# Kernel optimization log

Measured on AMD Instinct MI355X. Metric: run time of the kernel, lower is better.

The kernel has to match this reference:

```python
import jax, jax.numpy as jnp
import numpy as np

B, T, D, S, H = 512, 365, 16, 32, 256


def setup_inputs() -> dict:
    key = jax.random.key(0)
    ks = jax.random.split(key, 16)
    sc = 0.05
    rn = lambda k, shp: sc * jax.random.normal(k, shp, dtype=jnp.float32)
    return {
        "x": jax.random.normal(ks[0], (B, T, D), dtype=jnp.float32),
        "x_static": jax.random.normal(ks[1], (B, S), dtype=jnp.float32),
        # layer 0 LSTM params (PyTorch layout: [4H, in], gate order i,f,g,o)
        "Wih0": rn(ks[2], (4 * H, D)),
        "Whh0": rn(ks[3], (4 * H, H)),
        "bih0": rn(ks[4], (4 * H,)),
        "bhh0": rn(ks[5], (4 * H,)),
        # layer 1 LSTM params
        "Wih1": rn(ks[6], (4 * H, H)),
        "Whh1": rn(ks[7], (4 * H, H)),
        "bih1": rn(ks[8], (4 * H,)),
        "bhh1": rn(ks[9], (4 * H,)),
        # static_to_hidden Linear
        "Ws": rn(ks[10], (H, S)),
        "bs": rn(ks[11], (H,)),
        # output Linear (H -> 1)
        "Wo": rn(ks[12], (1, H)),
        "bo": rn(ks[13], (1,)),
    }


def _lstm_layer(x, h0, c0, Wih, Whh, bih, bhh):
    # Precompute input contribution as one big GEMM: [B,T,4H]
    xg = jnp.einsum('btd,gd->btg', x, Wih) + (bih + bhh)

    def step(carry, xt):
        h, c = carry
        g = xt + h @ Whh.T                      # [B,4H]
        i, f, gg, o = jnp.split(g, 4, axis=-1)  # PyTorch gate order i,f,g,o
        i = jax.nn.sigmoid(i)
        f = jax.nn.sigmoid(f)
        gg = jnp.tanh(gg)
        o = jax.nn.sigmoid(o)
        c = f * c + i * gg
        h = o * jnp.tanh(c)
        return (h, c), h

    (_, _), hs = jax.lax.scan(step, (h0, c0), jnp.swapaxes(xg, 0, 1))  # hs: [T,B,H]
    return jnp.swapaxes(hs, 0, 1)  # [B,T,H]


def reference(x, x_static, Wih0, Whh0, bih0, bhh0, Wih1, Whh1, bih1, bhh1, Ws, bs, Wo, bo):
    # h0 = c0 = static projection, shared across layers (repeat over num_layers)
    h0 = x_static @ Ws.T + bs                       # [B,H]
    y = _lstm_layer(x, h0, h0, Wih0, Whh0, bih0, bhh0)
    y = _lstm_layer(y, h0, h0, Wih1, Whh1, bih1, bhh1)
    out = (y @ Wo.T + bo)[..., 0]                   # [B,T]
    return out
```

## Files before the change

### kernel.cpp

```cpp
#include <hip/hip_runtime.h>

#define TT 365
#define BB 512
#define DD 16
#define HH 256
#define SS 32

typedef __attribute__((ext_vector_type(8))) short short8;
typedef __attribute__((ext_vector_type(4))) float f32x4;
typedef __attribute__((ext_vector_type(4))) unsigned u32x4;
typedef unsigned long long u64;

#define SENT 0x7FC07FC07FC07FC0ULL
#define TMASK64 0x4000400040004000ULL

__device__ __host__ inline short f2bf(float f){
  union { float f; unsigned u; } v; v.f = f;
  unsigned r = v.u + 0x7FFFu + ((v.u >> 16) & 1u);
  return (short)(r >> 16);
}
__device__ inline float sigm(float x){ return 1.0f/(1.0f+__expf(-x)); }
__device__ inline float tanhx(float x){ return 2.0f/(1.0f+__expf(-2.0f*x)) - 1.0f; }

__device__ inline unsigned cvtpk(float a, float b){
  unsigned r;
  asm("v_cvt_pk_bf16_f32 %0, %1, %2" : "=v"(r) : "v"(a), "v"(b));
  return r;
}

__device__ inline int fragAddr(int k, int m){
  return ((k>>5)*512) + ((((k&31)>>3)*16 + m)*8) + (k&7);
}

__device__ inline void pub_store(u64* p, u64 v){
  asm volatile("global_store_dwordx2 %0, %1, off sc0 sc1"
               :: "v"(p), "v"(v) : "memory");
}

#define RAW_BAR() do{ \
    asm volatile("s_waitcnt lgkmcnt(0)\n\ts_barrier" ::: "memory"); \
    __builtin_amdgcn_sched_barrier(0); }while(0)

__global__ void prep_weights(const float* __restrict__ Wih0, const float* __restrict__ Whh0,
                             const float* __restrict__ Wih1, const float* __restrict__ Whh1,
                             short* __restrict__ Wb0, short* __restrict__ Wb1)
{
  int idx = blockIdx.x*blockDim.x + threadIdx.x;
  const int n0 = 16*36*512;
  const int n1 = 16*64*512;
  if (idx < n0){
    int frag = idx >> 9, pos = idx & 511;
    int lane = pos >> 3, jj = pos & 7;
    int slot = frag / 36, rem = frag % 36;
    int ks = rem >> 2, nt = rem & 3;
    int n = nt*256 + slot*16 + (lane & 15);
    float v = 0.0f;
    if (ks == 0){
      int k32 = (lane>>4)*8 + jj;
      if (k32 < 16) v = Wih0[n*16 + k32];
    } else {
      int k = (ks-1)*32 + (lane>>4)*8 + jj;
      v = Whh0[n*256 + k];
    }
    Wb0[idx] = f2bf(v);
  } else if (idx < n0 + n1){
    int e = idx - n0;
    int frag = e >> 9, pos = e & 511;
    int lane = pos >> 3, jj = pos & 7;
    int slot = frag >> 6, rem = frag & 63;
    int ks = rem >> 2, nt = rem & 3;
    int n = nt*256 + slot*16 + (lane & 15);
    int k = ks*32 + (lane>>4)*8 + jj;
    float v = (k < 256) ? Wih1[n*256 + k] : Whh1[n*256 + (k-256)];
    Wb1[e] = f2bf(v);
  }
}

__global__ void prep_h0(const float* __restrict__ xs, const float* __restrict__ Ws,
                        const float* __restrict__ bs, float* __restrict__ h0init)
{
  int i = blockIdx.x*blockDim.x + threadIdx.x;
  int b = i >> 8, jj = i & 255;
  float s = bs[jj];
  const float* xr = xs + b*SS;
  const float* wr = Ws + jj*SS;
#pragma unroll
  for (int q=0;q<SS;++q) s += xr[q]*wr[q];
  h0init[i] = s;
}

__global__ void prep_bias(const float* __restrict__ a0, const float* __restrict__ a1,
                          const float* __restrict__ a2, const float* __restrict__ a3,
                          float* __restrict__ b0o, float* __restrict__ b1o)
{
  int i = threadIdx.x + blockIdx.x*blockDim.x;
  if (i < 1024) b0o[i] = a0[i] + a1[i];
  else if (i < 2048) b1o[i-1024] = a2[i-1024] + a3[i-1024];
}

__global__ void prep_zero(float* __restrict__ out, u64* __restrict__ ring)
{
  int i = blockIdx.x*blockDim.x + threadIdx.x;
  if (i < BB*TT) out[i] = 0.0f;
  if (i < 131072) ring[i] = SENT;
}

__global__ __launch_bounds__(256, 1) void lstm_fused(
    const short* __restrict__ Wb0, const short* __restrict__ Wb1,
    const float* __restrict__ h0i, const float* __restrict__ b0c,
    const float* __restrict__ b1c, const float* __restrict__ x,
    const float* __restrict__ Wo, const float* __restrict__ bo,
    u64* __restrict__ ring, float* __restrict__ out)
{
  __shared__ alignas(16) short AX[2][512];
  __shared__ alignas(16) short AH0[2][4096];
  __shared__ alignas(16) short AH1[4096];
  __shared__ float outacc[2][16][4];

  const int tid  = threadIdx.x;
  const int w    = tid >> 6;
  const int lane = tid & 63;
  const int col16= lane & 15;
  const int quad = lane >> 4;
  const int c    = blockIdx.x >> 5;
  const int g    = blockIdx.x & 31;
  const int rowbase = g * 16;
  const int slot = c*4 + w;
  const int colg = slot*16 + col16;

  short8 F0[36], F1[64];
  {
    const short8* p0 = (const short8*)Wb0 + slot*36*64 + lane;
#pragma unroll
    for (int f=0; f<36; ++f) F0[f] = p0[f*64];
    const short8* p1 = (const short8*)Wb1 + slot*64*64 + lane;
#pragma unroll
    for (int f=0; f<64; ++f) F1[f] = p1[f*64];
  }
  float bia0[4], bia1[4];
#pragma unroll
  for (int nt=0; nt<4; ++nt){
    bia0[nt] = b0c[nt*256 + slot*16 + col16];
    bia1[nt] = b1c[nt*256 + slot*16 + col16];
  }
  const float wo = Wo[colg];
  const float bos = bo[0];

  float c0[4], c1[4];
#pragma unroll
  for (int r=0; r<4; ++r){
    c0[r] = h0i[(rowbase + quad*4 + r)*HH + colg];
    c1[r] = c0[r];
  }
  for (int i = tid; i < 4096; i += 256){
    int m = i >> 8, k = i & 255;
    short v = f2bf(h0i[(rowbase+m)*HH + k]);
    int a = fragAddr(k,m);
    AH0[0][a] = v;
    AH1[a]    = v;
  }
  {
    int m = tid >> 4, d = tid & 15;
    AX[0][fragAddr(d, m)] = f2bf(x[(rowbase+m)*TT*DD + d]);
    AX[0][fragAddr(16 + d, m)] = 0;
    AX[1][fragAddr(16 + d, m)] = 0;
  }
  __syncthreads();

  const f32x4 zero = {0.0f,0.0f,0.0f,0.0f};
  const int qd = tid & 3;
  const int cl = (tid >> 2) & 63;
  const int ka = (((c + 1) & 3) << 6) + cl;
  const int kb = (((c + 2) & 3) << 6) + cl;
  const int kc = (((c + 3) & 3) << 6) + cl;

  u64 pv1_prev = 0;

#define CHKW(tv,dst,fl,TG) do{ u64 _t=(tv); \
    if(!(fl) && ((_t & TMASK64)==(TG))){ (dst)=_t & ~TMASK64; (fl)=true; } }while(0)

  for (int s=0; s<=TT; ++s){
    const bool doL0 = (s < TT);
    const bool doL1 = (s >= 1);
    const bool doH1x = (s >= 2);
    const int  p = s & 1;
    const unsigned T0 = (s>>1)&3;
    const unsigned w32_0 = ((T0&1)?0x4000u:0u) | ((T0&2)?0x40000000u:0u);
    const u64 tg0 = ((u64)w32_0<<32)|w32_0;
    const int  q1 = (s-1)&1;
    const unsigned T1 = ((s-1)>>1)&3;
    const unsigned w32_1 = ((T1&1)?0x4000u:0u) | ((T1&2)?0x40000000u:0u);
    const u64 tg1 = ((u64)w32_1<<32)|w32_1;

    short* ax   = AX[p];   short* ah0   = AH0[p];
    short* ax_n = AX[p^1]; short* ah0_n = AH0[p^1];
    u64* rb0 = ring + (p*32+g)*2048;
    u64* rb1 = ring + (q1*32+g)*2048;
    u64* P0a = rb0 + (ka*4+qd)*2;
    u64* P0b = rb0 + (kb*4+qd)*2;
    u64* P0c = rb0 + (kc*4+qd)*2;
    u64* P1a = rb1 + (ka*4+qd)*2 + 1;
    u64* P1b = rb1 + (kb*4+qd)*2 + 1;
    u64* P1c = rb1 + (kc*4+qd)*2 + 1;

    RAW_BAR();

    if (doH1x && tid < 16){
      float v = outacc[p^1][tid][0] + outacc[p^1][tid][1]
              + outacc[p^1][tid][2] + outacc[p^1][tid][3];
      if (c == 0) v += bos;
      atomicAdd(&out[(rowbase + tid)*TT + (s-2)], v);
    }

    float xf = 0.0f;
    if (s+1 < TT){
      int m = tid >> 4, d = tid & 15;
      xf = x[(rowbase+m)*TT*DD + (s+1)*DD + d];
    }

    u64 e1a=0, e1b=0, e1c=0;
    if (doH1x){
      asm volatile(
        "global_load_dwordx2 %0, %3, off sc0 sc1\n\t"
        "global_load_dwordx2 %1, %4, off sc0 sc1\n\t"
        "global_load_dwordx2 %2, %5, off sc0 sc1"
        : "=&v"(e1a),"=&v"(e1b),"=&v"(e1c)
        : "v"(P1a),"v"(P1b),"v"(P1c) : "memory");
    }

    u64 pv0 = 0;
    if (doL0){
      f32x4 acc0[4];
#pragma unroll
      for (int nt=0; nt<4; ++nt) acc0[nt] = zero;
      {
        short8 a = *(const short8*)(ax + lane*8);
#pragma unroll
        for (int nt=0; nt<4; ++nt)
          acc0[nt] = __builtin_amdgcn_mfma_f32_16x16x32_bf16(a, F0[nt], acc0[nt], 0,0,0);
      }
#pragma unroll
      for (int ks=0; ks<8; ++ks){
        short8 a = *(const short8*)(ah0 + ks*512 + lane*8);
#pragma unroll
        for (int nt=0; nt<4; ++nt)
          acc0[nt] = __builtin_amdgcn_mfma_f32_16x16x32_bf16(a, F0[(ks+1)*4+nt], acc0[nt], 0,0,0);
      }
      float h0v[4];
#pragma unroll
      for (int r=0; r<4; ++r){
        float iv = sigm (acc0[0][r] + bia0[0]);
        float fv = sigm (acc0[1][r] + bia0[1]);
        float gv = tanhx(acc0[2][r] + bia0[2]);
        float ov = sigm (acc0[3][r] + bia0[3]);
        float cc = fv*c0[r] + iv*gv;
        c0[r] = cc;
        h0v[r] = ov * tanhx(cc);
      }
      pv0 = (((u64)cvtpk(h0v[2], h0v[3])) << 32) | cvtpk(h0v[0], h0v[1]);
      pub_store(rb0 + (colg*4+quad)*2, pv0 | tg0);
#pragma unroll
      for (int r=0; r<4; ++r)
        ah0_n[fragAddr(colg, quad*4 + r)] = (short)(pv0 >> (16*r));
    }

    f32x4 acc1[4];
#pragma unroll
    for (int nt=0; nt<4; ++nt) acc1[nt] = zero;
    if (doL1){
#pragma unroll
      for (int ks=0; ks<8; ++ks){
        short8 a = *(const short8*)(ah0 + ks*512 + lane*8);
#pragma unroll
        for (int nt=0; nt<4; ++nt)
          acc1[nt] = __builtin_amdgcn_mfma_f32_16x16x32_bf16(a, F1[ks*4+nt], acc1[nt], 0,0,0);
      }
    }

    if (doH1x){
      __builtin_amdgcn_sched_barrier(0);
      if (doL0) asm volatile("s_waitcnt vmcnt(1)" ::: "memory");
      else      asm volatile("s_waitcnt vmcnt(0)" ::: "memory");
      __builtin_amdgcn_sched_barrier(0);
      u64 w1a=0,w1b=0,w1c=0;
      bool f1a=false,f1b=false,f1c=false;
      CHKW(e1a, w1a, f1a, tg1); CHKW(e1b, w1b, f1b, tg1); CHKW(e1c, w1c, f1c, tg1);
      while (!(f1a & f1b & f1c)){
        u64 t0,t1,t2;
        asm volatile(
          "global_load_dwordx2 %0, %3, off sc0 sc1\n\t"
          "global_load_dwordx2 %1, %4, off sc0 sc1\n\t"
          "global_load_dwordx2 %2, %5, off sc0 sc1\n\t"
          "s_waitcnt vmcnt(0)"
          : "=&v"(t0),"=&v"(t1),"=&v"(t2)
          : "v"(P1a),"v"(P1b),"v"(P1c) : "memory");
        __builtin_amdgcn_sched_barrier(0);
        CHKW(t0, w1a, f1a, tg1); CHKW(t1, w1b, f1b, tg1); CHKW(t2, w1c, f1c, tg1);
      }
#pragma unroll
      for (int r=0; r<4; ++r)
        AH1[fragAddr(colg, quad*4 + r)] = (short)(pv1_prev >> (16*r));
      {
        short* sv = (short*)&w1a;
#pragma unroll
        for (int r=0; r<4; ++r) AH1[fragAddr(ka, qd*4 + r)] = sv[r];
        sv = (short*)&w1b;
#pragma unroll
        for (int r=0; r<4; ++r) AH1[fragAddr(kb, qd*4 + r)] = sv[r];
        sv = (short*)&w1c;
#pragma unroll
        for (int r=0; r<4; ++r) AH1[fragAddr(kc, qd*4 + r)] = sv[r];
      }
    }

    u64 e0a=0, e0b=0, e0c=0;
    if (doL0){
      asm volatile(
        "global_load_dwordx2 %0, %3, off sc0 sc1\n\t"
        "global_load_dwordx2 %1, %4, off sc0 sc1\n\t"
        "global_load_dwordx2 %2, %5, off sc0 sc1"
        : "=&v"(e0a),"=&v"(e0b),"=&v"(e0c)
        : "v"(P0a),"v"(P0b),"v"(P0c) : "memory");
    }

    RAW_BAR();

    u64 pv1 = 0;
    if (doL1){
#pragma unroll
      for (int ks=0; ks<8; ++ks){
        short8 a = *(const short8*)(AH1 + ks*512 + lane*8);
#pragma unroll
        for (int nt=0; nt<4; ++nt)
          acc1[nt] = __builtin_amdgcn_mfma_f32_16x16x32_bf16(a, F1[32+ks*4+nt], acc1[nt], 0,0,0);
      }
      float pr[4], h1v[4];
#pragma unroll
      for (int r=0; r<4; ++r){
        float iv = sigm (acc1[0][r] + bia1[0]);
        float fv = sigm (acc1[1][r] + bia1[1]);
        float gv = tanhx(acc1[2][r] + bia1[2]);
        float ov = sigm (acc1[3][r] + bia1[3]);
        float cc = fv*c1[r] + iv*gv;
        c1[r] = cc;
        float h = ov * tanhx(cc);
        h1v[r] = h;
        pr[r] = h * wo;
      }
      pv1 = (((u64)cvtpk(h1v[2], h1v[3])) << 32) | cvtpk(h1v[0], h1v[1]);
      if (doL0)
        pub_store(rb0 + (colg*4+quad)*2 + 1, pv1 | tg0);
#pragma unroll
      for (int m=1; m<16; m<<=1){
#pragma unroll
        for (int r=0; r<4; ++r) pr[r] += __shfl_xor(pr[r], m, 64);
      }
      if (col16 == 0){
#pragma unroll
        for (int r=0; r<4; ++r) outacc[p][quad*4 + r][w] = pr[r];
      }
    }

    if (doL0){
      __builtin_amdgcn_sched_barrier(0);
      if (doL1) asm volatile("s_waitcnt vmcnt(1)" ::: "memory");
      else      asm volatile("s_waitcnt vmcnt(0)" ::: "memory");
      __builtin_amdgcn_sched_barrier(0);
      u64 w0a=0,w0b=0,w0c=0;
      bool f0a=false,f0b=false,f0c=false;
      CHKW(e0a, w0a, f0a, tg0); CHKW(e0b, w0b, f0b, tg0); CHKW(e0c, w0c, f0c, tg0);
      while (!(f0a & f0b & f0c)){
        u64 t0,t1,t2;
        asm volatile(
          "global_load_dwordx2 %0, %3, off sc0 sc1\n\t"
          "global_load_dwordx2 %1, %4, off sc0 sc1\n\t"
          "global_load_dwordx2 %2, %5, off sc0 sc1\n\t"
          "s_waitcnt vmcnt(0)"
          : "=&v"(t0),"=&v"(t1),"=&v"(t2)
          : "v"(P0a),"v"(P0b),"v"(P0c) : "memory");
        __builtin_amdgcn_sched_barrier(0);
        CHKW(t0, w0a, f0a, tg0); CHKW(t1, w0b, f0b, tg0); CHKW(t2, w0c, f0c, tg0);
      }
      {
        short* sv = (short*)&w0a;
#pragma unroll
        for (int r=0; r<4; ++r) ah0_n[fragAddr(ka, qd*4 + r)] = sv[r];
        sv = (short*)&w0b;
#pragma unroll
        for (int r=0; r<4; ++r) ah0_n[fragAddr(kb, qd*4 + r)] = sv[r];
        sv = (short*)&w0c;
#pragma unroll
        for (int r=0; r<4; ++r) ah0_n[fragAddr(kc, qd*4 + r)] = sv[r];
      }
      if (s+1 < TT){
        int m = tid >> 4, d = tid & 15;
        ax_n[fragAddr(d, m)] = f2bf(xf);
      }
    }

    pv1_prev = pv1;
  }
#undef CHKW

  RAW_BAR();
  if (tid < 16){
    const int pf = TT & 1;
    float v = outacc[pf][tid][0] + outacc[pf][tid][1]
            + outacc[pf][tid][2] + outacc[pf][tid][3];
    if (c == 0) v += bos;
    atomicAdd(&out[(rowbase + tid)*TT + (TT-1)], v);
  }
}

extern "C" void kernel_launch(void* const* d_in, const int* in_sizes, int n_in,
                              void* d_out, int out_size, void* d_ws, size_t ws_size,
                              hipStream_t stream)
{
  const float* x    = (const float*)d_in[0];
  const float* xs   = (const float*)d_in[1];
  const float* Wih0 = (const float*)d_in[2];
  const float* Whh0 = (const float*)d_in[3];
  const float* bih0 = (const float*)d_in[4];
  const float* bhh0 = (const float*)d_in[5];
  const float* Wih1 = (const float*)d_in[6];
  const float* Whh1 = (const float*)d_in[7];
  const float* bih1 = (const float*)d_in[8];
  const float* bhh1 = (const float*)d_in[9];
  const float* Ws   = (const float*)d_in[10];
  const float* bs   = (const float*)d_in[11];
  const float* Wo   = (const float*)d_in[12];
  const float* bo   = (const float*)d_in[13];
  float* out = (float*)d_out;

  char* ws = (char*)d_ws;
  short*    Wb0   = (short*)(ws);
  short*    Wb1   = (short*)(ws + 589824);
  float*    h0i   = (float*)(ws + 1638400);
  float*    b0cp  = (float*)(ws + 2162688);
  float*    b1cp  = (float*)(ws + 2166784);
  u64*      ring  = (u64*)(ws + 2170880);

  int nswz = 16*36*512 + 16*64*512;
  hipLaunchKernelGGL(prep_weights, dim3((nswz+255)/256), dim3(256), 0, stream,
                     Wih0, Whh0, Wih1, Whh1, Wb0, Wb1);
  hipLaunchKernelGGL(prep_h0, dim3(512), dim3(256), 0, stream, xs, Ws, bs, h0i);
  hipLaunchKernelGGL(prep_bias, dim3(8), dim3(256), 0, stream, bih0, bhh0, bih1, bhh1, b0cp, b1cp);
  hipLaunchKernelGGL(prep_zero, dim3(1024), dim3(256), 0, stream, out, ring);

  hipLaunchKernelGGL(lstm_fused, dim3(128), dim3(256), 0, stream,
                     Wb0, Wb1, h0i, b0cp, b1cp, x, Wo, bo, ring, out);
}
```

Before: 1.577 ms.

## Concentrate cross-block ring polling in wave 0 with 16-byte loads

The global ring layout is split into separate layer-0 and layer-1 regions, so each lane's remote hidden-state chunk is contiguous. Only wave 0 now polls the ring for peer blocks' hidden states, using six dwordx4 loads per lane instead of all four waves issuing three dwordx2 loads each. The x-input prefetch becomes an explicit asm load with manual vmcnt accounting for the other waves, and the atomic output reduction moves to wave 1. The aim is to cut redundant global polling traffic and wait overhead on the latency-critical recurrent path. The cost is that wave 0 carries the whole spin-wait and LDS scatter, and the hand-tuned vmcnt counts are fragile.

```diff
diff --git a/kernel.cpp b/kernel.cpp
--- a/kernel.cpp
+++ b/kernel.cpp
@@ -40,6 +40,33 @@
 #define RAW_BAR() do{ \
     asm volatile("s_waitcnt lgkmcnt(0)\n\ts_barrier" ::: "memory"); \
     __builtin_amdgcn_sched_barrier(0); }while(0)
+
+#define ISSUE6(o0,o1,o2,o3,o4,o5,a0,a1,a2,a3,a4,a5) \
+  asm volatile( \
+    "global_load_dwordx4 %0, %6, off sc0 sc1\n\t" \
+    "global_load_dwordx4 %1, %7, off sc0 sc1\n\t" \
+    "global_load_dwordx4 %2, %8, off sc0 sc1\n\t" \
+    "global_load_dwordx4 %3, %9, off sc0 sc1\n\t" \
+    "global_load_dwordx4 %4, %10, off sc0 sc1\n\t" \
+    "global_load_dwordx4 %5, %11, off sc0 sc1" \
+    : "=&v"(o0),"=&v"(o1),"=&v"(o2),"=&v"(o3),"=&v"(o4),"=&v"(o5) \
+    : "v"(a0),"v"(a1),"v"(a2),"v"(a3),"v"(a4),"v"(a5) : "memory")
+
+__device__ inline bool tok(u32x4 v, u64 tg){
+  u64 lo = (((u64)v.y)<<32)|v.x, hi = (((u64)v.w)<<32)|v.z;
+  return ((lo & TMASK64) == tg) && ((hi & TMASK64) == tg);
+}
+
+__device__ inline void wrx4(short* arr, int cP, int j, int lane, u32x4 v){
+  int k  = cP*64 + j*32 + (lane>>1);
+  int q0 = (lane&1)*2;
+  u64 lo = ((((u64)v.y)<<32)|v.x) & ~TMASK64;
+  u64 hi = ((((u64)v.w)<<32)|v.z) & ~TMASK64;
+#pragma unroll
+  for (int r=0;r<4;++r) arr[fragAddr(k, q0*4+r)]     = (short)(lo>>(16*r));
+#pragma unroll
+  for (int r=0;r<4;++r) arr[fragAddr(k, (q0+1)*4+r)] = (short)(hi>>(16*r));
+}
 
 __global__ void prep_weights(const float* __restrict__ Wih0, const float* __restrict__ Whh0,
                              const float* __restrict__ Wih1, const float* __restrict__ Whh1,
@@ -127,6 +154,7 @@
   const int rowbase = g * 16;
   const int slot = c*4 + w;
   const int colg = slot*16 + col16;
+  const bool w0  = (w == 0);
 
   short8 F0[36], F1[64];
   {
@@ -168,16 +196,9 @@
   __syncthreads();
 
   const f32x4 zero = {0.0f,0.0f,0.0f,0.0f};
-  const int qd = tid & 3;
-  const int cl = (tid >> 2) & 63;
-  const int ka = (((c + 1) & 3) << 6) + cl;
-  const int kb = (((c + 2) & 3) << 6) + cl;
-  const int kc = (((c + 3) & 3) << 6) + cl;
+  const int ca = (c+1)&3, cb = (c+2)&3, cc2 = (c+3)&3;
 
   u64 pv1_prev = 0;
-
-#define CHKW(tv,dst,fl,TG) do{ u64 _t=(tv); \
-    if(!(fl) && ((_t & TMASK64)==(TG))){ (dst)=_t & ~TMASK64; (fl)=true; } }while(0)
 
   for (int s=0; s<=TT; ++s){
     const bool doL0 = (s < TT);
@@ -187,45 +208,39 @@
     const unsigned T0 = (s>>1)&3;
     const unsigned w32_0 = ((T0&1)?0x4000u:0u) | ((T0&2)?0x40000000u:0u);
     const u64 tg0 = ((u64)w32_0<<32)|w32_0;
-    const int  q1 = (s-1)&1;
     const unsigned T1 = ((s-1)>>1)&3;
     const unsigned w32_1 = ((T1&1)?0x4000u:0u) | ((T1&2)?0x40000000u:0u);
     const u64 tg1 = ((u64)w32_1<<32)|w32_1;
 
     short* ax   = AX[p];   short* ah0   = AH0[p];
     short* ax_n = AX[p^1]; short* ah0_n = AH0[p^1];
-    u64* rb0 = ring + (p*32+g)*2048;
-    u64* rb1 = ring + (q1*32+g)*2048;
-    u64* P0a = rb0 + (ka*4+qd)*2;
-    u64* P0b = rb0 + (kb*4+qd)*2;
-    u64* P0c = rb0 + (kc*4+qd)*2;
-    u64* P1a = rb1 + (ka*4+qd)*2 + 1;
-    u64* P1b = rb1 + (kb*4+qd)*2 + 1;
-    u64* P1c = rb1 + (kc*4+qd)*2 + 1;
+    u64* const rgn0 = ring + (u64)(p*32+g)*2048;
+    u64* const rgn1 = ring + (u64)(((s-1)&1)*32+g)*2048;
+
+    const u64* A0 = rgn1 + 1024 + ca *256 + lane*2;  const u64* A1 = A0 + 128;
+    const u64* B0p= rgn1 + 1024 + cb *256 + lane*2;  const u64* B1p= B0p + 128;
+    const u64* C0p= rgn1 + 1024 + cc2*256 + lane*2;  const u64* C1p= C0p + 128;
+    const u64* D0 = rgn0 + ca *256 + lane*2;         const u64* D1 = D0 + 128;
+    const u64* E0 = rgn0 + cb *256 + lane*2;         const u64* E1 = E0 + 128;
+    const u64* G0 = rgn0 + cc2*256 + lane*2;         const u64* G1 = G0 + 128;
 
     RAW_BAR();
 
-    if (doH1x && tid < 16){
-      float v = outacc[p^1][tid][0] + outacc[p^1][tid][1]
-              + outacc[p^1][tid][2] + outacc[p^1][tid][3];
+    if (doH1x && tid >= 64 && tid < 80){
+      int row = tid - 64;
+      float v = outacc[p^1][row][0] + outacc[p^1][row][1]
+              + outacc[p^1][row][2] + outacc[p^1][row][3];
       if (c == 0) v += bos;
-      atomicAdd(&out[(rowbase + tid)*TT + (s-2)], v);
-    }
+      atomicAdd(&out[(rowbase + row)*TT + (s-2)], v);
+    }
+
+    u32x4 ya0,ya1,yb0,yb1,yc0,yc1;
+    if (w0 && doH1x){ ISSUE6(ya0,ya1,yb0,yb1,yc0,yc1, A0,A1,B0p,B1p,C0p,C1p); }
 
     float xf = 0.0f;
     if (s+1 < TT){
-      int m = tid >> 4, d = tid & 15;
-      xf = x[(rowbase+m)*TT*DD + (s+1)*DD + d];
-    }
-
-    u64 e1a=0, e1b=0, e1c=0;
-    if (doH1x){
-      asm volatile(
-        "global_load_dwordx2 %0, %3, off sc0 sc1\n\t"
-        "global_load_dwordx2 %1, %4, off sc0 sc1\n\t"
-        "global_load_dwordx2 %2, %5, off sc0 sc1"
-        : "=&v"(e1a),"=&v"(e1b),"=&v"(e1c)
-        : "v"(P1a),"v"(P1b),"v"(P1c) : "memory");
+      const float* xp = x + (rowbase+(tid>>4))*TT*DD + (s+1)*DD + (tid&15);
+      asm volatile("global_load_dword %0, %1, off" : "=&v"(xf) : "v"(xp) : "memory");
     }
 
     u64 pv0 = 0;
@@ -258,7 +273,7 @@
         h0v[r] = ov * tanhx(cc);
       }
       pv0 = (((u64)cvtpk(h0v[2], h0v[3])) << 32) | cvtpk(h0v[0], h0v[1]);
-      pub_store(rb0 + (colg*4+quad)*2, pv0 | tg0);
+      pub_store(rgn0 + colg*4 + quad, pv0 | tg0);
 #pragma unroll
       for (int r=0; r<4; ++r)
         ah0_n[fragAddr(colg, quad*4 + r)] = (short)(pv0 >> (16*r));
@@ -277,51 +292,29 @@
       }
     }
 
-    if (doH1x){
+    if (w0 && doH1x){
       __builtin_amdgcn_sched_barrier(0);
-      if (doL0) asm volatile("s_waitcnt vmcnt(1)" ::: "memory");
+      if (doL0) asm volatile("s_waitcnt vmcnt(2)" ::: "memory");
       else      asm volatile("s_waitcnt vmcnt(0)" ::: "memory");
       __builtin_amdgcn_sched_barrier(0);
-      u64 w1a=0,w1b=0,w1c=0;
-      bool f1a=false,f1b=false,f1c=false;
-      CHKW(e1a, w1a, f1a, tg1); CHKW(e1b, w1b, f1b, tg1); CHKW(e1c, w1c, f1c, tg1);
-      while (!(f1a & f1b & f1c)){
-        u64 t0,t1,t2;
-        asm volatile(
-          "global_load_dwordx2 %0, %3, off sc0 sc1\n\t"
-          "global_load_dwordx2 %1, %4, off sc0 sc1\n\t"
-          "global_load_dwordx2 %2, %5, off sc0 sc1\n\t"
-          "s_waitcnt vmcnt(0)"
-          : "=&v"(t0),"=&v"(t1),"=&v"(t2)
-          : "v"(P1a),"v"(P1b),"v"(P1c) : "memory");
+      while (!(tok(ya0,tg1)&&tok(ya1,tg1)&&tok(yb0,tg1)&&
+               tok(yb1,tg1)&&tok(yc0,tg1)&&tok(yc1,tg1))){
+        ISSUE6(ya0,ya1,yb0,yb1,yc0,yc1, A0,A1,B0p,B1p,C0p,C1p);
+        asm volatile("s_waitcnt vmcnt(0)" ::: "memory");
         __builtin_amdgcn_sched_barrier(0);
-        CHKW(t0, w1a, f1a, tg1); CHKW(t1, w1b, f1b, tg1); CHKW(t2, w1c, f1c, tg1);
-      }
+      }
+      wrx4(AH1, ca, 0, lane, ya0);  wrx4(AH1, ca, 1, lane, ya1);
+      wrx4(AH1, cb, 0, lane, yb0);  wrx4(AH1, cb, 1, lane, yb1);
+      wrx4(AH1, cc2,0, lane, yc0);  wrx4(AH1, cc2,1, lane, yc1);
+    }
+    if (doH1x){
 #pragma unroll
       for (int r=0; r<4; ++r)
         AH1[fragAddr(colg, quad*4 + r)] = (short)(pv1_prev >> (16*r));
-      {
-        short* sv = (short*)&w1a;
-#pragma unroll
-        for (int r=0; r<4; ++r) AH1[fragAddr(ka, qd*4 + r)] = sv[r];
-        sv = (short*)&w1b;
-#pragma unroll
-        for (int r=0; r<4; ++r) AH1[fragAddr(kb, qd*4 + r)] = sv[r];
-        sv = (short*)&w1c;
-#pragma unroll
-        for (int r=0; r<4; ++r) AH1[fragAddr(kc, qd*4 + r)] = sv[r];
-      }
-    }
-
-    u64 e0a=0, e0b=0, e0c=0;
-    if (doL0){
-      asm volatile(
-        "global_load_dwordx2 %0, %3, off sc0 sc1\n\t"
-        "global_load_dwordx2 %1, %4, off sc0 sc1\n\t"
-        "global_load_dwordx2 %2, %5, off sc0 sc1"
-        : "=&v"(e0a),"=&v"(e0b),"=&v"(e0c)
-        : "v"(P0a),"v"(P0b),"v"(P0c) : "memory");
-    }
+    }
+
+    u32x4 za0,za1,zb0,zb1,zc0,zc1;
+    if (w0 && doL0){ ISSUE6(za0,za1,zb0,zb1,zc0,zc1, D0,D1,E0,E1,G0,G1); }
 
     RAW_BAR();
 
@@ -349,7 +342,7 @@
       }
       pv1 = (((u64)cvtpk(h1v[2], h1v[3])) << 32) | cvtpk(h1v[0], h1v[1]);
       if (doL0)
-        pub_store(rb0 + (colg*4+quad)*2 + 1, pv1 | tg0);
+        pub_store(rgn0 + 1024 + colg*4 + quad, pv1 | tg0);
 #pragma unroll
       for (int m=1; m<16; m<<=1){
 #pragma unroll
@@ -361,54 +354,41 @@
       }
     }
 
-    if (doL0){
+    if (w0 && doL0){
       __builtin_amdgcn_sched_barrier(0);
       if (doL1) asm volatile("s_waitcnt vmcnt(1)" ::: "memory");
       else      asm volatile("s_waitcnt vmcnt(0)" ::: "memory");
       __builtin_amdgcn_sched_barrier(0);
-      u64 w0a=0,w0b=0,w0c=0;
-      bool f0a=false,f0b=false,f0c=false;
-      CHKW(e0a, w0a, f0a, tg0); CHKW(e0b, w0b, f0b, tg0); CHKW(e0c, w0c, f0c, tg0);
-      while (!(f0a & f0b & f0c)){
-        u64 t0,t1,t2;
-        asm volatile(
-          "global_load_dwordx2 %0, %3, off sc0 sc1\n\t"
-          "global_load_dwordx2 %1, %4, off sc0 sc1\n\t"
-          "global_load_dwordx2 %2, %5, off sc0 sc1\n\t"
-          "s_waitcnt vmcnt(0)"
-          : "=&v"(t0),"=&v"(t1),"=&v"(t2)
-          : "v"(P0a),"v"(P0b),"v"(P0c) : "memory");
+      while (!(tok(za0,tg0)&&tok(za1,tg0)&&tok(zb0,tg0)&&
+               tok(zb1,tg0)&&tok(zc0,tg0)&&tok(zc1,tg0))){
+        ISSUE6(za0,za1,zb0,zb1,zc0,zc1, D0,D1,E0,E1,G0,G1);
+        asm volatile("s_waitcnt vmcnt(0)" ::: "memory");
         __builtin_amdgcn_sched_barrier(0);
-        CHKW(t0, w0a, f0a, tg0); CHKW(t1, w0b, f0b, tg0); CHKW(t2, w0c, f0c, tg0);
-      }
-      {
-        short* sv = (short*)&w0a;
-#pragma unroll
-        for (int r=0; r<4; ++r) ah0_n[fragAddr(ka, qd*4 + r)] = sv[r];
-        sv = (short*)&w0b;
-#pragma unroll
-        for (int r=0; r<4; ++r) ah0_n[fragAddr(kb, qd*4 + r)] = sv[r];
-        sv = (short*)&w0c;
-#pragma unroll
-        for (int r=0; r<4; ++r) ah0_n[fragAddr(kc, qd*4 + r)] = sv[r];
-      }
-      if (s+1 < TT){
-        int m = tid >> 4, d = tid & 15;
-        ax_n[fragAddr(d, m)] = f2bf(xf);
-      }
+      }
+      wrx4(ah0_n, ca, 0, lane, za0);  wrx4(ah0_n, ca, 1, lane, za1);
+      wrx4(ah0_n, cb, 0, lane, zb0);  wrx4(ah0_n, cb, 1, lane, zb1);
+      wrx4(ah0_n, cc2,0, lane, zc0);  wrx4(ah0_n, cc2,1, lane, zc1);
+    }
+    if (s+1 < TT){
+      if (!w0){
+        if (s == 0) asm volatile("s_waitcnt vmcnt(1)" ::: "memory");
+        else        asm volatile("s_waitcnt vmcnt(2)" ::: "memory");
+        __builtin_amdgcn_sched_barrier(0);
+      }
+      ax_n[fragAddr(tid & 15, tid >> 4)] = f2bf(xf);
     }
 
     pv1_prev = pv1;
   }
-#undef CHKW
 
   RAW_BAR();
-  if (tid < 16){
+  if (tid >= 64 && tid < 80){
+    int row = tid - 64;
     const int pf = TT & 1;
-    float v = outacc[pf][tid][0] + outacc[pf][tid][1]
-            + outacc[pf][tid][2] + outacc[pf][tid][3];
+    float v = outacc[pf][row][0] + outacc[pf][row][1]
+            + outacc[pf][row][2] + outacc[pf][row][3];
     if (c == 0) v += bos;
-    atomicAdd(&out[(rowbase + tid)*TT + (TT-1)], v);
+    atomicAdd(&out[(rowbase + row)*TT + (TT-1)], v);
   }
 }
 
```

Result: slower. 2.633 ms (+67.0%).

## Issue layer-0 exchange loads mid layer-1 MFMA and prefetch x asynchronously

Applied to the files above, without the earlier changes.

Splits the layer-1 input-side MFMA loop in two and issues the cross-block layer-0 hidden-state polling loads between the halves. This starts the exchange latency earlier and hides it behind matrix work. The next-step x value is now fetched with an inline-asm load, and it is written to LDS only after an explicit vmcnt wait. The waitcnt values are retuned to match the new order of memory operations. The output atomic moves from wave 0 to wave 1 to take it off the critical wave. The hand-counted vmcnt values are fragile and depend on exactly how many loads and stores are in flight.

```diff
diff --git a/kernel.cpp b/kernel.cpp
--- a/kernel.cpp
+++ b/kernel.cpp
@@ -8,7 +8,6 @@
 
 typedef __attribute__((ext_vector_type(8))) short short8;
 typedef __attribute__((ext_vector_type(4))) float f32x4;
-typedef __attribute__((ext_vector_type(4))) unsigned u32x4;
 typedef unsigned long long u64;
 
 #define SENT 0x7FC07FC07FC07FC0ULL
@@ -187,15 +186,14 @@
     const unsigned T0 = (s>>1)&3;
     const unsigned w32_0 = ((T0&1)?0x4000u:0u) | ((T0&2)?0x40000000u:0u);
     const u64 tg0 = ((u64)w32_0<<32)|w32_0;
-    const int  q1 = (s-1)&1;
     const unsigned T1 = ((s-1)>>1)&3;
     const unsigned w32_1 = ((T1&1)?0x4000u:0u) | ((T1&2)?0x40000000u:0u);
     const u64 tg1 = ((u64)w32_1<<32)|w32_1;
 
     short* ax   = AX[p];   short* ah0   = AH0[p];
     short* ax_n = AX[p^1]; short* ah0_n = AH0[p^1];
-    u64* rb0 = ring + (p*32+g)*2048;
-    u64* rb1 = ring + (q1*32+g)*2048;
+    u64* rb0 = ring + (u64)(p*32+g)*2048;
+    u64* rb1 = ring + (u64)(((s-1)&1)*32+g)*2048;
     u64* P0a = rb0 + (ka*4+qd)*2;
     u64* P0b = rb0 + (kb*4+qd)*2;
     u64* P0c = rb0 + (kc*4+qd)*2;
@@ -205,17 +203,12 @@
 
     RAW_BAR();
 
-    if (doH1x && tid < 16){
-      float v = outacc[p^1][tid][0] + outacc[p^1][tid][1]
-              + outacc[p^1][tid][2] + outacc[p^1][tid][3];
+    if (doH1x && tid >= 64 && tid < 80){
+      int row = tid - 64;
+      float v = outacc[p^1][row][0] + outacc[p^1][row][1]
+              + outacc[p^1][row][2] + outacc[p^1][row][3];
       if (c == 0) v += bos;
-      atomicAdd(&out[(rowbase + tid)*TT + (s-2)], v);
-    }
-
-    float xf = 0.0f;
-    if (s+1 < TT){
-      int m = tid >> 4, d = tid & 15;
-      xf = x[(rowbase+m)*TT*DD + (s+1)*DD + d];
+      atomicAdd(&out[(rowbase + row)*TT + (s-2)], v);
     }
 
     u64 e1a=0, e1b=0, e1c=0;
@@ -228,6 +221,13 @@
         : "v"(P1a),"v"(P1b),"v"(P1c) : "memory");
     }
 
+    float xf = 0.0f;
+    if (doL0){
+      int sx = (s+1 < TT) ? s+1 : TT-1;
+      const float* xp = x + (rowbase+(tid>>4))*TT*DD + sx*DD + (tid&15);
+      asm volatile("global_load_dword %0, %1, off" : "=&v"(xf) : "v"(xp) : "memory");
+    }
+
     u64 pv0 = 0;
     if (doL0){
       f32x4 acc0[4];
@@ -269,7 +269,7 @@
     for (int nt=0; nt<4; ++nt) acc1[nt] = zero;
     if (doL1){
 #pragma unroll
-      for (int ks=0; ks<8; ++ks){
+      for (int ks=0; ks<4; ++ks){
         short8 a = *(const short8*)(ah0 + ks*512 + lane*8);
 #pragma unroll
         for (int nt=0; nt<4; ++nt)
@@ -277,9 +277,29 @@
       }
     }
 
+    u64 e0a=0, e0b=0, e0c=0;
+    if (doL0){
+      asm volatile(
+        "global_load_dwordx2 %0, %3, off sc0 sc1\n\t"
+        "global_load_dwordx2 %1, %4, off sc0 sc1\n\t"
+        "global_load_dwordx2 %2, %5, off sc0 sc1"
+        : "=&v"(e0a),"=&v"(e0b),"=&v"(e0c)
+        : "v"(P0a),"v"(P0b),"v"(P0c) : "memory");
+    }
+
+    if (doL1){
+#pragma unroll
+      for (int ks=4; ks<8; ++ks){
+        short8 a = *(const short8*)(ah0 + ks*512 + lane*8);
+#pragma unroll
+        for (int nt=0; nt<4; ++nt)
+          acc1[nt] = __builtin_amdgcn_mfma_f32_16x16x32_bf16(a, F1[ks*4+nt], acc1[nt], 0,0,0);
+      }
+    }
+
     if (doH1x){
       __builtin_amdgcn_sched_barrier(0);
-      if (doL0) asm volatile("s_waitcnt vmcnt(1)" ::: "memory");
+      if (doL0) asm volatile("s_waitcnt vmcnt(5)" ::: "memory");
       else      asm volatile("s_waitcnt vmcnt(0)" ::: "memory");
       __builtin_amdgcn_sched_barrier(0);
       u64 w1a=0,w1b=0,w1c=0;
@@ -313,16 +333,6 @@
       }
     }
 
-    u64 e0a=0, e0b=0, e0c=0;
-    if (doL0){
-      asm volatile(
-        "global_load_dwordx2 %0, %3, off sc0 sc1\n\t"
-        "global_load_dwordx2 %1, %4, off sc0 sc1\n\t"
-        "global_load_dwordx2 %2, %5, off sc0 sc1"
-        : "=&v"(e0a),"=&v"(e0b),"=&v"(e0c)
-        : "v"(P0a),"v"(P0b),"v"(P0c) : "memory");
-    }
-
     RAW_BAR();
 
     u64 pv1 = 0;
@@ -363,6 +373,11 @@
 
     if (doL0){
       __builtin_amdgcn_sched_barrier(0);
+      asm volatile("s_waitcnt vmcnt(4)" ::: "memory");
+      __builtin_amdgcn_sched_barrier(0);
+      if (s+1 < TT)
+        ax_n[fragAddr(tid & 15, tid >> 4)] = f2bf(xf);
+
       if (doL1) asm volatile("s_waitcnt vmcnt(1)" ::: "memory");
       else      asm volatile("s_waitcnt vmcnt(0)" ::: "memory");
       __builtin_amdgcn_sched_barrier(0);
@@ -392,10 +407,6 @@
 #pragma unroll
         for (int r=0; r<4; ++r) ah0_n[fragAddr(kc, qd*4 + r)] = sv[r];
       }
-      if (s+1 < TT){
-        int m = tid >> 4, d = tid & 15;
-        ax_n[fragAddr(d, m)] = f2bf(xf);
-      }
     }
 
     pv1_prev = pv1;
```

Result: faster. 1.508 ms (-4.4%).
